# Kernel optimization log

Hardware: AMD Instinct MI355X
Metric: run time of the kernel (lower is better)

Reference implementation:

```python
import jax, jax.numpy as jnp
import numpy as np

HEAD_DIM = 128
PATCH = (1, 2, 2)
MAX_SEQ = 1024
THETA = 10000.0
FIXED_REF = 30
H_DIM = 2 * (HEAD_DIM // 6)          # 42
W_DIM = 2 * (HEAD_DIM // 6)          # 42
T_DIM = HEAD_DIM - H_DIM - W_DIM     # 44


def _rope_1d(dim, max_seq_len, theta):
    # matches get_1d_rotary_pos_embed(use_real=True, repeat_interleave_real=True)
    inv = 1.0 / (theta ** (jnp.arange(0, dim, 2, dtype=jnp.float32) / dim))  # [dim/2]
    ang = jnp.arange(max_seq_len, dtype=jnp.float32)[:, None] * inv[None, :]  # [S, dim/2]
    cos = jnp.repeat(jnp.cos(ang), 2, axis=1)  # [S, dim]
    sin = jnp.repeat(jnp.sin(ang), 2, axis=1)
    return cos, sin


def setup_inputs() -> dict:
    key = jax.random.key(0)
    hs = jax.random.normal(key, (1, 16, 22, 120, 120), dtype=jnp.float32)
    t_cos, t_sin = _rope_1d(T_DIM, MAX_SEQ, THETA)
    h_cos, h_sin = _rope_1d(H_DIM, MAX_SEQ, THETA)
    w_cos, w_sin = _rope_1d(W_DIM, MAX_SEQ, THETA)
    return {
        "hidden_states": hs,
        "freq_t_cos": t_cos, "freq_h_cos": h_cos, "freq_w_cos": w_cos,
        "freq_t_sin": t_sin, "freq_h_sin": h_sin, "freq_w_sin": w_sin,
        "num_video_frames": 21,
        "num_ref_frames": 1,
    }


def _build(t_tab, h_tab, w_tab, pos_t, height, width):
    F = pos_t.shape[0]
    t = t_tab[pos_t]                 # [F, T_DIM]
    h = h_tab[:height]               # [height, H_DIM]
    w = w_tab[:width]                # [width, W_DIM]
    grid = jnp.concatenate([
        jnp.broadcast_to(t[:, None, None, :], (F, height, width, T_DIM)),
        jnp.broadcast_to(h[None, :, None, :], (F, height, width, H_DIM)),
        jnp.broadcast_to(w[None, None, :, :], (F, height, width, W_DIM)),
    ], axis=-1)                      # [F, height, width, HEAD_DIM]
    return grid.reshape(1, F * height * width, 1, HEAD_DIM)


def reference(hidden_states, freq_t_cos, freq_h_cos, freq_w_cos,
              freq_t_sin, freq_h_sin, freq_w_sin,
              num_video_frames, num_ref_frames):
    _, _, _, H, W = hidden_states.shape
    p_t, p_h, p_w = PATCH
    height, width = H // p_h, W // p_w
    video_pp = num_video_frames // p_t
    ref_pp = num_ref_frames // p_t
    # temporal positions: sequential for video frames, fixed 30 for ref frames
    pos_t = jnp.concatenate([
        jnp.arange(video_pp, dtype=jnp.int32),
        jnp.full((ref_pp,), FIXED_REF, dtype=jnp.int32),
    ])
    freqs_cos = _build(freq_t_cos, freq_h_cos, freq_w_cos, pos_t, height, width)
    freqs_sin = _build(freq_t_sin, freq_h_sin, freq_w_sin, pos_t, height, width)
    return freqs_cos, freqs_sin
```

## Files before the change

kernel.cpp:

```cpp
#include <hip/hip_runtime.h>


#define RP_T_DIM 44
#define RP_H_DIM 42
#define RP_W_DIM 42
#define RP_HEAD_DIM 128
#define RP_FIXED_REF 30

__global__ __launch_bounds__(256) void wan_rope_kernel(
    const float* __restrict__ t_cos, const float* __restrict__ h_cos,
    const float* __restrict__ w_cos, const float* __restrict__ t_sin,
    const float* __restrict__ h_sin, const float* __restrict__ w_sin,
    const int* __restrict__ nvf_ptr,
    float* __restrict__ out,
    int height, int width, long long sin_offset)
{
    const int rows_per_frame = height * width;
    const int quads_per_frame = rows_per_frame * (RP_HEAD_DIM / 4);
    const int tid = blockIdx.x * blockDim.x + threadIdx.x;
    if (tid >= quads_per_frame) return;

    const int f   = blockIdx.y;
    const int row = tid >> 5;
    const int d0  = (tid & 31) << 2;
    const int y   = row / width;
    const int x   = row - y * width;

    const int video_pp = nvf_ptr[0];
    const int pos = (f < video_pp) ? f : RP_FIXED_REF;

    float cv[4], sv[4];
#pragma unroll
    for (int j = 0; j < 4; ++j) {
        const int d = d0 + j;
        float cc, ss;
        if (d < RP_T_DIM) {
            cc = t_cos[pos * RP_T_DIM + d];
            ss = t_sin[pos * RP_T_DIM + d];
        } else if (d < RP_T_DIM + RP_H_DIM) {
            const int dd = d - RP_T_DIM;
            cc = h_cos[y * RP_H_DIM + dd];
            ss = h_sin[y * RP_H_DIM + dd];
        } else {
            const int dd = d - RP_T_DIM - RP_H_DIM;
            cc = w_cos[x * RP_W_DIM + dd];
            ss = w_sin[x * RP_W_DIM + dd];
        }
        cv[j] = cc;
        sv[j] = ss;
    }

    const long long base =
        ((long long)f * rows_per_frame + row) * RP_HEAD_DIM + d0;
    *(float4*)(out + base) = make_float4(cv[0], cv[1], cv[2], cv[3]);
    *(float4*)(out + sin_offset + base) = make_float4(sv[0], sv[1], sv[2], sv[3]);
}

extern "C" void kernel_launch(void* const* d_in, const int* in_sizes, int n_in,
                              void* d_out, int out_size, void* d_ws, size_t ws_size,
                              hipStream_t stream) {
    const float* t_cos = (const float*)d_in[1];
    const float* h_cos = (const float*)d_in[2];
    const float* w_cos = (const float*)d_in[3];
    const float* t_sin = (const float*)d_in[4];
    const float* h_sin = (const float*)d_in[5];
    const float* w_sin = (const float*)d_in[6];
    const int*   nvf   = (const int*)d_in[7];
    float* out = (float*)d_out;

    const int height = 60, width = 60;

    const long long per_out = (long long)out_size / 2;
    const int F = (int)(per_out / ((long long)height * width * RP_HEAD_DIM));

    const int quads_per_frame = height * width * (RP_HEAD_DIM / 4);
    dim3 block(256);
    dim3 grid((quads_per_frame + 255) / 256, F);
    wan_rope_kernel<<<grid, block, 0, stream>>>(
        t_cos, h_cos, w_cos, t_sin, h_sin, w_sin, nvf,
        out, height, width, per_out);
}
```

Before: 118.2 us.

## Stage per-row rope tables in LDS with aligned padded layout for vector reads

Result: faster. 111.4 us (-5.7%).

```diff
diff --git a/kernel.cpp b/kernel.cpp
--- a/kernel.cpp
+++ b/kernel.cpp
@@ -4,56 +4,72 @@
 #define RP_T_DIM 44
 #define RP_H_DIM 42
 #define RP_W_DIM 42
-#define RP_HEAD_DIM 128
+#define RP_HEAD 128
+#define RP_GH 60
+#define RP_GW 60
 #define RP_FIXED_REF 30
+#define RP_TH 86
+#define RP_TH_PAD 88
+#define RP_WROW 44
+#define RP_LDS_FLOATS (RP_TH_PAD + RP_GW * RP_WROW)
 
-__global__ __launch_bounds__(256) void wan_rope_kernel(
+#define RP_BLOCK 320
+
+__global__ __launch_bounds__(RP_BLOCK) void wan_rope_kernel(
     const float* __restrict__ t_cos, const float* __restrict__ h_cos,
     const float* __restrict__ w_cos, const float* __restrict__ t_sin,
     const float* __restrict__ h_sin, const float* __restrict__ w_sin,
     const int* __restrict__ nvf_ptr,
-    float* __restrict__ out,
-    int height, int width, long long sin_offset)
+    float* __restrict__ out, long long sin_offset)
 {
-    const int rows_per_frame = height * width;
-    const int quads_per_frame = rows_per_frame * (RP_HEAD_DIM / 4);
-    const int tid = blockIdx.x * blockDim.x + threadIdx.x;
-    if (tid >= quads_per_frame) return;
+    __shared__ __align__(16) float lds_c[RP_LDS_FLOATS];
+    __shared__ __align__(16) float lds_s[RP_LDS_FLOATS];
 
-    const int f   = blockIdx.y;
-    const int row = tid >> 5;
-    const int d0  = (tid & 31) << 2;
-    const int y   = row / width;
-    const int x   = row - y * width;
+    const int tid = threadIdx.x;
+    const int y = blockIdx.x;
+    const int f = blockIdx.y;
 
-    const int video_pp = nvf_ptr[0];
-    const int pos = (f < video_pp) ? f : RP_FIXED_REF;
+    const int vpp = nvf_ptr[0];
+    const int pos = (f < vpp) ? f : RP_FIXED_REF;
 
-    float cv[4], sv[4];
-#pragma unroll
-    for (int j = 0; j < 4; ++j) {
-        const int d = d0 + j;
-        float cc, ss;
-        if (d < RP_T_DIM) {
-            cc = t_cos[pos * RP_T_DIM + d];
-            ss = t_sin[pos * RP_T_DIM + d];
-        } else if (d < RP_T_DIM + RP_H_DIM) {
-            const int dd = d - RP_T_DIM;
-            cc = h_cos[y * RP_H_DIM + dd];
-            ss = h_sin[y * RP_H_DIM + dd];
-        } else {
-            const int dd = d - RP_T_DIM - RP_H_DIM;
-            cc = w_cos[x * RP_W_DIM + dd];
-            ss = w_sin[x * RP_W_DIM + dd];
-        }
-        cv[j] = cc;
-        sv[j] = ss;
+    if (tid < RP_T_DIM) {
+        lds_c[tid] = t_cos[pos * RP_T_DIM + tid];
+        lds_s[tid] = t_sin[pos * RP_T_DIM + tid];
+    } else if (tid < RP_TH) {
+        const int j = tid - RP_T_DIM;
+        lds_c[tid] = h_cos[y * RP_H_DIM + j];
+        lds_s[tid] = h_sin[y * RP_H_DIM + j];
     }
 
-    const long long base =
-        ((long long)f * rows_per_frame + row) * RP_HEAD_DIM + d0;
-    *(float4*)(out + base) = make_float4(cv[0], cv[1], cv[2], cv[3]);
-    *(float4*)(out + sin_offset + base) = make_float4(sv[0], sv[1], sv[2], sv[3]);
+    for (int i = tid; i < 2 * RP_GW; i += RP_BLOCK) {
+        const int x = i >> 1, j = i & 1;
+        lds_c[RP_TH_PAD + x * RP_WROW + j] = h_cos[y * RP_H_DIM + 40 + j];
+        lds_s[RP_TH_PAD + x * RP_WROW + j] = h_sin[y * RP_H_DIM + 40 + j];
+    }
+
+    for (int sIdx = tid; sIdx < RP_GW * RP_W_DIM; sIdx += RP_BLOCK) {
+        const int x = sIdx / RP_W_DIM;
+        const int j = sIdx - x * RP_W_DIM;
+        lds_c[RP_TH_PAD + x * RP_WROW + 2 + j] = w_cos[sIdx];
+        lds_s[RP_TH_PAD + x * RP_WROW + 2 + j] = w_sin[sIdx];
+    }
+
+    __syncthreads();
+
+    const long long rowbase = (long long)f * (RP_GH * RP_GW) + y * RP_GW;
+#pragma unroll
+    for (int it = 0; it < 6; ++it) {
+        const int flat = it * RP_BLOCK + tid;
+        const int x = flat >> 5;
+        const int q = flat & 31;
+        const int lidx = (q < 21) ? (q << 2)
+                                  : (RP_TH_PAD + x * RP_WROW + ((q - 21) << 2));
+        const float4 c = *(const float4*)(lds_c + lidx);
+        const float4 s = *(const float4*)(lds_s + lidx);
+        const long long base = (rowbase + x) * RP_HEAD + (q << 2);
+        *(float4*)(out + base) = c;
+        *(float4*)(out + sin_offset + base) = s;
+    }
 }
 
 extern "C" void kernel_launch(void* const* d_in, const int* in_sizes, int n_in,
@@ -68,15 +84,11 @@
     const int*   nvf   = (const int*)d_in[7];
     float* out = (float*)d_out;
 
-    const int height = 60, width = 60;
+    const long long per_out = (long long)out_size / 2;
+    const int F = (int)(per_out / ((long long)RP_GH * RP_GW * RP_HEAD));
 
-    const long long per_out = (long long)out_size / 2;
-    const int F = (int)(per_out / ((long long)height * width * RP_HEAD_DIM));
-
-    const int quads_per_frame = height * width * (RP_HEAD_DIM / 4);
-    dim3 block(256);
-    dim3 grid((quads_per_frame + 255) / 256, F);
+    dim3 block(RP_BLOCK);
+    dim3 grid(RP_GH, F);
     wan_rope_kernel<<<grid, block, 0, stream>>>(
-        t_cos, h_cos, w_cos, t_sin, h_sin, w_sin, nvf,
-        out, height, width, per_out);
+        t_cos, h_cos, w_cos, t_sin, h_sin, w_sin, nvf, out, per_out);
 }
```
